# Kernel optimization log

Hardware: AMD Instinct MI355X
Metric: run time of the kernel (lower is better)

The kernel has to match this reference:

```python
import jax, jax.numpy as jnp
import numpy as np

N_NODES = 100000
N_EDGES = 1600000
D_IN = 128
D_HID = 64


def setup_inputs() -> dict:
    key = jax.random.key(0)
    k1, k2, k3, k4 = jax.random.split(key, 4)
    x = jax.random.normal(k1, (N_NODES, D_IN), dtype=jnp.float32)
    edge_index = jax.random.randint(k2, (2, N_EDGES), 0, N_NODES, dtype=jnp.int64)
    W1 = jax.random.normal(k3, (D_IN, D_HID), dtype=jnp.float32) / np.sqrt(D_IN)
    b1 = jnp.zeros((D_HID,), dtype=jnp.float32)
    W2 = jax.random.normal(k4, (D_HID, 1), dtype=jnp.float32) / np.sqrt(D_HID)
    b2 = jnp.zeros((1,), dtype=jnp.float32)
    return {"x": x, "edge_index": edge_index, "W1": W1, "b1": b1, "W2": W2, "b2": b2}


def _gcn_layer(x, W, b, src, dst, norm, n):
    # PyG GCNConv: linear transform, then normalized scatter-add aggregation, then bias
    h = x @ W                                   # [N, d_out]
    msg = h[src] * norm[:, None]                # gather + edge-weight   [E', d_out]
    out = jax.ops.segment_sum(msg, dst, num_segments=n)  # scatter-add
    return out + b


def reference(x, edge_index, W1, b1, W2, b2):
    n = x.shape[0]
    loops = jnp.arange(n, dtype=edge_index.dtype)
    src = jnp.concatenate([edge_index[0], loops])  # self-loops added (GCN default)
    dst = jnp.concatenate([edge_index[1], loops])
    # symmetric normalization: deg^{-1/2}[src] * deg^{-1/2}[dst]
    deg = jax.ops.segment_sum(jnp.ones(dst.shape, x.dtype), dst, num_segments=n)
    dis = jnp.where(deg > 0, jax.lax.rsqrt(jnp.maximum(deg, 1e-12)), 0.0)
    norm = dis[src] * dis[dst]
    h = jax.nn.relu(_gcn_layer(x, W1, b1, src, dst, norm, n))
    y = _gcn_layer(h, W2, b2, src, dst, norm, n)   # [N, 1]
    # ConstantPad1d((0, num_node_features-1), 0) -> [N, D_IN]
    return jnp.pad(y, ((0, 0), (0, x.shape[1] - 1)))
```

## Files before the change

### kernel.cpp

```cpp
#include <hip/hip_runtime.h>

#define N_NODES 100000
#define N_EDGES 1600000
#define D_IN 128
#define D_HID 64

#define BKT_SHIFT 8
#define BKT_NODES 256
#define NB 391
#define NBLK 392
#define SLOT 32
#define SEG4 (SLOT / 4)
#define REG4 (NBLK * SEG4)
#define BKT_CAP 5120
#define OVF_CAP 8192

typedef __attribute__((ext_vector_type(8))) short bf16x8;
typedef __attribute__((ext_vector_type(4))) float f32x4;

__device__ __forceinline__ unsigned short f2b(float f) {
    union { float f; unsigned u; } c; c.f = f;
    unsigned r = (c.u + 0x7FFFu + ((c.u >> 16) & 1u)) >> 16;
    return (unsigned short)r;
}
__device__ __forceinline__ float blo(unsigned u) { return __uint_as_float(u << 16); }
__device__ __forceinline__ float bhi(unsigned u) { return __uint_as_float(u & 0xffff0000u); }

__global__ __launch_bounds__(256) void k_prep(const float* __restrict__ W1,
                                              unsigned short* __restrict__ w1t,
                                              int* __restrict__ ovf_cnt) {
    int t = blockIdx.x * 256 + threadIdx.x;
    if (t == 0) ovf_cnt[0] = 0;
    int k = t >> 6, f = t & 63;
    w1t[f * D_IN + k] = f2b(W1[t]);
}

__global__ __launch_bounds__(256) void k_escatter(const int* __restrict__ src,
                                                  const int* __restrict__ dst,
                                                  int* __restrict__ pairs,
                                                  int* __restrict__ cnt_blk,
                                                  int* __restrict__ ovf_cnt,
                                                  int2* __restrict__ ovf, int E) {
    __shared__ int lcur[NB];
    int tid = threadIdx.x;
    for (int t = tid; t < NB; t += 256) lcur[t] = 0;
    __syncthreads();
    int chunk = (E + NBLK - 1) / NBLK;
    int beg = blockIdx.x * chunk;
    int end = min(beg + chunk, E);
    for (int e = beg + tid; e < end; e += 256) {
        int d = dst[e], s = src[e];
        int bk = d >> BKT_SHIFT;
        int slot = atomicAdd(&lcur[bk], 1);
        if (slot < SLOT)
            pairs[(bk * NBLK + blockIdx.x) * SLOT + slot] = (s << BKT_SHIFT) | (d & (BKT_NODES - 1));
        else {
            int o = atomicAdd(ovf_cnt, 1);
            if (o < OVF_CAP) ovf[o] = make_int2(s, d);
        }
    }
    __syncthreads();
    for (int t = tid; t < NB; t += 256)
        cnt_blk[t * NBLK + blockIdx.x] = min(lcur[t], SLOT);
}

__global__ __launch_bounds__(256) void k_bsort(const uint4* __restrict__ pairs4,
                                               const int* __restrict__ cnt_blk,
                                               const int* __restrict__ ovf_cnt,
                                               const int2* __restrict__ ovf,
                                               int* __restrict__ srcs_sorted,
                                               int* __restrict__ row_start,
                                               int* __restrict__ row_end,
                                               float* __restrict__ dis, int n) {
    __shared__ int segc[NBLK];
    __shared__ int cnt[BKT_NODES];
    __shared__ int exc[BKT_NODES];
    __shared__ int sorted[BKT_CAP];
    __shared__ int nE_sh;
    int b = blockIdx.x;
    int tid = threadIdx.x;
    int node0 = b << BKT_SHIFT;
    int ocnt = min(ovf_cnt[0], OVF_CAP);
    const uint4* region = pairs4 + (size_t)b * REG4;

    for (int i = tid; i < NBLK; i += 256) segc[i] = cnt_blk[b * NBLK + i];
    cnt[tid] = 0;
    __syncthreads();

    for (int i4 = tid; i4 < REG4; i4 += 256) {
        uint4 v = region[i4];
        int c = segc[i4 >> 3];
        int k = (i4 & 7) * 4;
        if (k < c)     atomicAdd(&cnt[v.x & (BKT_NODES - 1)], 1);
        if (k + 1 < c) atomicAdd(&cnt[v.y & (BKT_NODES - 1)], 1);
        if (k + 2 < c) atomicAdd(&cnt[v.z & (BKT_NODES - 1)], 1);
        if (k + 3 < c) atomicAdd(&cnt[v.w & (BKT_NODES - 1)], 1);
    }
    for (int k = tid; k < ocnt; k += 256) {
        int2 e = ovf[k];
        if ((e.y >> BKT_SHIFT) == b) atomicAdd(&cnt[e.y & (BKT_NODES - 1)], 1);
    }
    __syncthreads();

    if (tid < 64) {
        int run = 0;
        for (int c = 0; c < BKT_NODES; c += 64) {
            int v = cnt[c + tid];
            int inc = v;
            for (int off = 1; off < 64; off <<= 1) {
                int t2 = __shfl_up(inc, off);
                if (tid >= off) inc += t2;
            }
            exc[c + tid] = run + inc - v;
            run += __shfl(inc, 63);
        }
        if (tid == 63) nE_sh = run;
    }
    __syncthreads();

    int node = node0 + tid;
    if (node < n) {
        int rs = b * BKT_CAP + exc[tid];
        row_start[node] = rs;
        row_end[node] = rs + cnt[tid];
        dis[node] = rsqrtf((float)cnt[tid] + 1.0f);
    }
    int nE = nE_sh;
    __syncthreads();
    cnt[tid] = exc[tid];
    __syncthreads();

    for (int i4 = tid; i4 < REG4; i4 += 256) {
        uint4 v = region[i4];
        int c = segc[i4 >> 3];
        int k = (i4 & 7) * 4;
        if (k < c)     { int p = atomicAdd(&cnt[v.x & (BKT_NODES - 1)], 1); sorted[p] = v.x >> BKT_SHIFT; }
        if (k + 1 < c) { int p = atomicAdd(&cnt[v.y & (BKT_NODES - 1)], 1); sorted[p] = v.y >> BKT_SHIFT; }
        if (k + 2 < c) { int p = atomicAdd(&cnt[v.z & (BKT_NODES - 1)], 1); sorted[p] = v.z >> BKT_SHIFT; }
        if (k + 3 < c) { int p = atomicAdd(&cnt[v.w & (BKT_NODES - 1)], 1); sorted[p] = v.w >> BKT_SHIFT; }
    }
    for (int k = tid; k < ocnt; k += 256) {
        int2 e = ovf[k];
        if ((e.y >> BKT_SHIFT) == b) {
            int p = atomicAdd(&cnt[e.y & (BKT_NODES - 1)], 1);
            sorted[p] = e.x;
        }
    }
    __syncthreads();

    int gbase = b * BKT_CAP;
    for (int k = tid; k < nE; k += 256)
        srcs_sorted[gbase + k] = sorted[k];
}

#define LS 136
__global__ __launch_bounds__(256) void k_gemm1(const float* __restrict__ x,
                                               const uint4* __restrict__ w1t4,
                                               const float* __restrict__ dis,
                                               unsigned short* __restrict__ h1s, int n) {
    __shared__ unsigned short xs[64 * LS];
    __shared__ unsigned short ws[64 * LS];
    int tid = threadIdx.x;
    int node0 = blockIdx.x * 64;

#pragma unroll
    for (int it = 0; it < 4; ++it) {
        int e = tid + it * 256;
        int f = e >> 4, c = e & 15;
        *(uint4*)&ws[f * LS + c * 8] = w1t4[e];
    }
#pragma unroll
    for (int it = 0; it < 8; ++it) {
        int e4 = tid + it * 256;
        int node = e4 >> 5;
        int k = (e4 & 31) * 4;
        float4 v = make_float4(0.f, 0.f, 0.f, 0.f);
        if (node0 + node < n)
            v = ((const float4*)x)[((size_t)(node0 + node) * D_IN + k) >> 2];
        uint2 u;
        u.x = (unsigned)f2b(v.x) | ((unsigned)f2b(v.y) << 16);
        u.y = (unsigned)f2b(v.z) | ((unsigned)f2b(v.w) << 16);
        *(uint2*)&xs[node * LS + k] = u;
    }
    __syncthreads();

    int wv = tid >> 6;
    int lane = tid & 63;
    int m16 = lane & 15;
    int q = lane >> 4;

    bf16x8 afrag[4];
#pragma unroll
    for (int ks = 0; ks < 4; ++ks)
        afrag[ks] = *(const bf16x8*)&xs[(wv * 16 + m16) * LS + ks * 32 + q * 8];

    f32x4 acc[4];
#pragma unroll
    for (int ft = 0; ft < 4; ++ft) acc[ft] = (f32x4){0.f, 0.f, 0.f, 0.f};

#pragma unroll
    for (int ft = 0; ft < 4; ++ft)
#pragma unroll
        for (int ks = 0; ks < 4; ++ks) {
            bf16x8 bfrag = *(const bf16x8*)&ws[(ft * 16 + m16) * LS + ks * 32 + q * 8];
            acc[ft] = __builtin_amdgcn_mfma_f32_16x16x32_bf16(afrag[ks], bfrag, acc[ft], 0, 0, 0);
        }

#pragma unroll
    for (int r = 0; r < 4; ++r) {
        int node = node0 + wv * 16 + q * 4 + r;
        if (node < n) {
            float d = dis[node];
#pragma unroll
            for (int ft = 0; ft < 4; ++ft)
                h1s[(size_t)node * D_HID + ft * 16 + m16] = f2b(acc[ft][r] * d);
        }
    }
}

__global__ __launch_bounds__(256) void k_gather1(const int* __restrict__ srcs,
                                                 const int* __restrict__ row_start,
                                                 const int* __restrict__ row_end,
                                                 const float* __restrict__ dis,
                                                 const uint4* __restrict__ h4,
                                                 const float* __restrict__ b1,
                                                 const float* __restrict__ W2,
                                                 float* __restrict__ zd, int n) {
    int i = blockIdx.x * 8 + (threadIdx.x >> 5);
    int lane = threadIdx.x & 63;
    int g = (lane >> 3) & 3;
    int m8 = lane & 7;
    float dd = dis[i];

    float a0, a1, a2, a3, a4, a5, a6, a7;
    {
        uint4 u = h4[(unsigned)i * 8u + m8];
        float w = (g == 0) ? 1.f : 0.f;
        a0 = w * blo(u.x); a1 = w * bhi(u.x);
        a2 = w * blo(u.y); a3 = w * bhi(u.y);
        a4 = w * blo(u.z); a5 = w * bhi(u.z);
        a6 = w * blo(u.w); a7 = w * bhi(u.w);
    }

#define ACC(u) { a0 += blo(u.x); a1 += bhi(u.x); a2 += blo(u.y); a3 += bhi(u.y); \
                 a4 += blo(u.z); a5 += bhi(u.z); a6 += blo(u.w); a7 += bhi(u.w); }
    int end = row_end[i];
    int j = row_start[i] + g;
    for (; j + 4 < end; j += 8) {
        int s0 = srcs[j];
        int s1 = srcs[j + 4];
        uint4 u0 = h4[(unsigned)s0 * 8u + m8];
        uint4 u1 = h4[(unsigned)s1 * 8u + m8];
        ACC(u0); ACC(u1);
    }
    if (j < end) {
        int s0 = srcs[j];
        uint4 u0 = h4[(unsigned)s0 * 8u + m8];
        ACC(u0);
    }
#undef ACC

#pragma unroll
    for (int off = 8; off < 32; off <<= 1) {
        a0 += __shfl_xor(a0, off); a1 += __shfl_xor(a1, off);
        a2 += __shfl_xor(a2, off); a3 += __shfl_xor(a3, off);
        a4 += __shfl_xor(a4, off); a5 += __shfl_xor(a5, off);
        a6 += __shfl_xor(a6, off); a7 += __shfl_xor(a7, off);
    }
    float4 ba = ((const float4*)b1)[m8 * 2];
    float4 bb = ((const float4*)b1)[m8 * 2 + 1];
    float4 wa = ((const float4*)W2)[m8 * 2];
    float4 wb = ((const float4*)W2)[m8 * 2 + 1];
    float v = fmaxf(fmaf(dd, a0, ba.x), 0.f) * wa.x + fmaxf(fmaf(dd, a1, ba.y), 0.f) * wa.y
            + fmaxf(fmaf(dd, a2, ba.z), 0.f) * wa.z + fmaxf(fmaf(dd, a3, ba.w), 0.f) * wa.w
            + fmaxf(fmaf(dd, a4, bb.x), 0.f) * wb.x + fmaxf(fmaf(dd, a5, bb.y), 0.f) * wb.y
            + fmaxf(fmaf(dd, a6, bb.z), 0.f) * wb.z + fmaxf(fmaf(dd, a7, bb.w), 0.f) * wb.w;
#pragma unroll
    for (int off = 1; off < 8; off <<= 1) v += __shfl_xor(v, off);
    if ((lane & 31) == 0) zd[i] = v * dd;
}

__global__ __launch_bounds__(256) void k_gather2(const int* __restrict__ srcs,
                                                 const int* __restrict__ row_start,
                                                 const int* __restrict__ row_end,
                                                 const float* __restrict__ dis,
                                                 const float* __restrict__ zd,
                                                 const float* __restrict__ b2,
                                                 float* __restrict__ out, int n) {
    int i = blockIdx.x * 8 + (threadIdx.x >> 5);
    int l = threadIdx.x & 31;
    float acc = 0.f;
    int beg = row_start[i], end = row_end[i];
    for (int j = beg + l; j < end; j += 32)
        acc += zd[srcs[j]];
#pragma unroll
    for (int off = 1; off < 32; off <<= 1) acc += __shfl_xor(acc, off);
    float y = (acc + zd[i]) * dis[i] + b2[0];
    float4 v = make_float4(0.f, 0.f, 0.f, 0.f);
    if (l == 0) v.x = y;
    ((float4*)out)[(size_t)i * 32 + l] = v;
}

extern "C" void kernel_launch(void* const* d_in, const int* in_sizes, int n_in,
                              void* d_out, int out_size, void* d_ws, size_t ws_size,
                              hipStream_t stream) {
    const float* x  = (const float*)d_in[0];
    const int*   ei = (const int*)d_in[1];
    const float* W1 = (const float*)d_in[2];
    const float* b1 = (const float*)d_in[3];
    const float* W2 = (const float*)d_in[4];
    const float* b2 = (const float*)d_in[5];
    float* out = (float*)d_out;

    const int n = N_NODES;
    const int E = N_EDGES;
    const int* src = ei;
    const int* dst = ei + E;

    int* pairs       = (int*)d_ws;
    int* cnt_blk     = pairs + (size_t)NB * NBLK * SLOT;
    int* srcs_sorted = cnt_blk + (size_t)NB * NBLK;
    int* row_start   = srcs_sorted + (size_t)NB * BKT_CAP;
    int* row_end     = row_start + n;
    int* ovf_cnt     = row_end + n;
    int2* ovf        = (int2*)(ovf_cnt + 4);
    float* dis       = (float*)(ovf + OVF_CAP);
    unsigned short* h1s = (unsigned short*)(dis + n);
    unsigned short* w1t = h1s + (size_t)n * D_HID;
    float* zd        = (float*)(w1t + D_IN * D_HID);

    k_prep<<<32, 256, 0, stream>>>(W1, w1t, ovf_cnt);
    k_escatter<<<NBLK, 256, 0, stream>>>(src, dst, pairs, cnt_blk, ovf_cnt, ovf, E);
    k_bsort<<<NB, 256, 0, stream>>>((const uint4*)pairs, cnt_blk, ovf_cnt, ovf,
                                    srcs_sorted, row_start, row_end, dis, n);

    k_gemm1<<<(n + 63) / 64, 256, 0, stream>>>(x, (const uint4*)w1t, dis, h1s, n);

    k_gather1<<<(n + 7) / 8, 256, 0, stream>>>(srcs_sorted, row_start, row_end, dis,
                                               (const uint4*)h1s, b1, W2, zd, n);
    k_gather2<<<(n + 7) / 8, 256, 0, stream>>>(srcs_sorted, row_start, row_end, dis,
                                               zd, b2, out, n);
}
```

Baseline: 213.2 us.

## Stage bucket pairs compactly in LDS once and fold W1 prep into scatter

The bucket sort kernel now prefix-sums the per-block segment counts and reads the padded global pair region once, compacting only valid entries into a shared staging array. Both the count and placement passes then iterate over that dense array, so the second global read and the idle padded-slot work are gone. The separate W1 transpose kernel is merged into the edge scatter kernel, and the overflow counter is reset with a memset, which removes one kernel launch. In exchange the kernel uses an extra 20KB of LDS, which may reduce occupancy.

```diff
diff --git a/kernel.cpp b/kernel.cpp
--- a/kernel.cpp
+++ b/kernel.cpp
@@ -26,23 +26,21 @@
 __device__ __forceinline__ float blo(unsigned u) { return __uint_as_float(u << 16); }
 __device__ __forceinline__ float bhi(unsigned u) { return __uint_as_float(u & 0xffff0000u); }
 
-__global__ __launch_bounds__(256) void k_prep(const float* __restrict__ W1,
-                                              unsigned short* __restrict__ w1t,
-                                              int* __restrict__ ovf_cnt) {
-    int t = blockIdx.x * 256 + threadIdx.x;
-    if (t == 0) ovf_cnt[0] = 0;
-    int k = t >> 6, f = t & 63;
-    w1t[f * D_IN + k] = f2b(W1[t]);
-}
-
 __global__ __launch_bounds__(256) void k_escatter(const int* __restrict__ src,
                                                   const int* __restrict__ dst,
+                                                  const float* __restrict__ W1,
+                                                  unsigned short* __restrict__ w1t,
                                                   int* __restrict__ pairs,
                                                   int* __restrict__ cnt_blk,
                                                   int* __restrict__ ovf_cnt,
                                                   int2* __restrict__ ovf, int E) {
     __shared__ int lcur[NB];
     int tid = threadIdx.x;
+    if (blockIdx.x < 32) {
+        int t = blockIdx.x * 256 + tid;
+        int k = t >> 6, f = t & 63;
+        w1t[f * D_IN + k] = f2b(W1[t]);
+    }
     for (int t = tid; t < NB; t += 256) lcur[t] = 0;
     __syncthreads();
     int chunk = (E + NBLK - 1) / NBLK;
@@ -73,8 +71,10 @@
                                                int* __restrict__ row_end,
                                                float* __restrict__ dis, int n) {
     __shared__ int segc[NBLK];
+    __shared__ int segb[NBLK];
     __shared__ int cnt[BKT_NODES];
     __shared__ int exc[BKT_NODES];
+    __shared__ int staged[BKT_CAP];
     __shared__ int sorted[BKT_CAP];
     __shared__ int nE_sh;
     int b = blockIdx.x;
@@ -87,15 +87,41 @@
     cnt[tid] = 0;
     __syncthreads();
 
+    if (tid < 64) {
+        int run = 0;
+        for (int c = 0; c < NBLK; c += 64) {
+            int idx = c + tid;
+            int v = (idx < NBLK) ? segc[idx] : 0;
+            int inc = v;
+            for (int off = 1; off < 64; off <<= 1) {
+                int t2 = __shfl_up(inc, off);
+                if (tid >= off) inc += t2;
+            }
+            if (idx < NBLK) segb[idx] = run + inc - v;
+            run += __shfl(inc, 63);
+        }
+        if (tid == 63) nE_sh = run;
+    }
+    __syncthreads();
+
     for (int i4 = tid; i4 < REG4; i4 += 256) {
-        uint4 v = region[i4];
-        int c = segc[i4 >> 3];
+        int seg = i4 >> 3;
+        int c = segc[seg];
         int k = (i4 & 7) * 4;
-        if (k < c)     atomicAdd(&cnt[v.x & (BKT_NODES - 1)], 1);
-        if (k + 1 < c) atomicAdd(&cnt[v.y & (BKT_NODES - 1)], 1);
-        if (k + 2 < c) atomicAdd(&cnt[v.z & (BKT_NODES - 1)], 1);
-        if (k + 3 < c) atomicAdd(&cnt[v.w & (BKT_NODES - 1)], 1);
-    }
+        if (k < c) {
+            uint4 v = region[i4];
+            int base = segb[seg] + k;
+            if (base < BKT_CAP)                  staged[base]     = v.x;
+            if (k + 1 < c && base + 1 < BKT_CAP) staged[base + 1] = v.y;
+            if (k + 2 < c && base + 2 < BKT_CAP) staged[base + 2] = v.z;
+            if (k + 3 < c && base + 3 < BKT_CAP) staged[base + 3] = v.w;
+        }
+    }
+    __syncthreads();
+    int nE = min(nE_sh, BKT_CAP);
+
+    for (int k = tid; k < nE; k += 256)
+        atomicAdd(&cnt[staged[k] & (BKT_NODES - 1)], 1);
     for (int k = tid; k < ocnt; k += 256) {
         int2 e = ovf[k];
         if ((e.y >> BKT_SHIFT) == b) atomicAdd(&cnt[e.y & (BKT_NODES - 1)], 1);
@@ -114,30 +140,25 @@
             exc[c + tid] = run + inc - v;
             run += __shfl(inc, 63);
         }
-        if (tid == 63) nE_sh = run;
     }
     __syncthreads();
 
     int node = node0 + tid;
+    int tot = exc[BKT_NODES - 1] + cnt[BKT_NODES - 1];
     if (node < n) {
         int rs = b * BKT_CAP + exc[tid];
         row_start[node] = rs;
         row_end[node] = rs + cnt[tid];
         dis[node] = rsqrtf((float)cnt[tid] + 1.0f);
     }
-    int nE = nE_sh;
     __syncthreads();
     cnt[tid] = exc[tid];
     __syncthreads();
 
-    for (int i4 = tid; i4 < REG4; i4 += 256) {
-        uint4 v = region[i4];
-        int c = segc[i4 >> 3];
-        int k = (i4 & 7) * 4;
-        if (k < c)     { int p = atomicAdd(&cnt[v.x & (BKT_NODES - 1)], 1); sorted[p] = v.x >> BKT_SHIFT; }
-        if (k + 1 < c) { int p = atomicAdd(&cnt[v.y & (BKT_NODES - 1)], 1); sorted[p] = v.y >> BKT_SHIFT; }
-        if (k + 2 < c) { int p = atomicAdd(&cnt[v.z & (BKT_NODES - 1)], 1); sorted[p] = v.z >> BKT_SHIFT; }
-        if (k + 3 < c) { int p = atomicAdd(&cnt[v.w & (BKT_NODES - 1)], 1); sorted[p] = v.w >> BKT_SHIFT; }
+    for (int k = tid; k < nE; k += 256) {
+        int pk = staged[k];
+        int p = atomicAdd(&cnt[pk & (BKT_NODES - 1)], 1);
+        sorted[p] = pk >> BKT_SHIFT;
     }
     for (int k = tid; k < ocnt; k += 256) {
         int2 e = ovf[k];
@@ -149,7 +170,8 @@
     __syncthreads();
 
     int gbase = b * BKT_CAP;
-    for (int k = tid; k < nE; k += 256)
+    int nTot = min(tot, BKT_CAP);
+    for (int k = tid; k < nTot; k += 256)
         srcs_sorted[gbase + k] = sorted[k];
 }
 
@@ -329,8 +351,8 @@
     unsigned short* w1t = h1s + (size_t)n * D_HID;
     float* zd        = (float*)(w1t + D_IN * D_HID);
 
-    k_prep<<<32, 256, 0, stream>>>(W1, w1t, ovf_cnt);
-    k_escatter<<<NBLK, 256, 0, stream>>>(src, dst, pairs, cnt_blk, ovf_cnt, ovf, E);
+    hipMemsetAsync(ovf_cnt, 0, 4, stream);
+    k_escatter<<<NBLK, 256, 0, stream>>>(src, dst, W1, w1t, pairs, cnt_blk, ovf_cnt, ovf, E);
     k_bsort<<<NB, 256, 0, stream>>>((const uint4*)pairs, cnt_blk, ovf_cnt, ovf,
                                     srcs_sorted, row_start, row_end, dis, n);
 
```

Result: slower. 222.1 us (+4.2%).

## Fuse edge scatter and GEMM1 into one launch, apply source norm in gather

Applied to the files above, without the earlier changes.

Merges the edge-scatter kernel and the first dense GEMM into a single heterogeneous launch, so the GEMM blocks run alongside the scatter blocks. Because the GEMM now runs before degrees are known, it stores unscaled h1, and the gather kernel multiplies each neighbour row by dis[src] with an extra scalar load per edge. The W1 transpose/prep kernel is dropped: every GEMM block converts W1 itself, and the overflow counter is reset with a memset. Launch count and serialization go down, but the gather does extra random loads and each GEMM block does redundant W1 conversion with strided shared-memory stores.

```diff
diff --git a/kernel.cpp b/kernel.cpp
--- a/kernel.cpp
+++ b/kernel.cpp
@@ -9,6 +9,7 @@
 #define BKT_NODES 256
 #define NB 391
 #define NBLK 392
+#define GBLK 1563
 #define SLOT 32
 #define SEG4 (SLOT / 4)
 #define REG4 (NBLK * SEG4)
@@ -26,42 +27,98 @@
 __device__ __forceinline__ float blo(unsigned u) { return __uint_as_float(u << 16); }
 __device__ __forceinline__ float bhi(unsigned u) { return __uint_as_float(u & 0xffff0000u); }
 
-__global__ __launch_bounds__(256) void k_prep(const float* __restrict__ W1,
-                                              unsigned short* __restrict__ w1t,
-                                              int* __restrict__ ovf_cnt) {
-    int t = blockIdx.x * 256 + threadIdx.x;
-    if (t == 0) ovf_cnt[0] = 0;
-    int k = t >> 6, f = t & 63;
-    w1t[f * D_IN + k] = f2b(W1[t]);
-}
-
-__global__ __launch_bounds__(256) void k_escatter(const int* __restrict__ src,
-                                                  const int* __restrict__ dst,
-                                                  int* __restrict__ pairs,
-                                                  int* __restrict__ cnt_blk,
-                                                  int* __restrict__ ovf_cnt,
-                                                  int2* __restrict__ ovf, int E) {
+#define LS 136
+__global__ __launch_bounds__(256) void k_build(const int* __restrict__ src,
+                                               const int* __restrict__ dst,
+                                               const float* __restrict__ x,
+                                               const float* __restrict__ W1,
+                                               int* __restrict__ pairs,
+                                               int* __restrict__ cnt_blk,
+                                               int* __restrict__ ovf_cnt,
+                                               int2* __restrict__ ovf,
+                                               unsigned short* __restrict__ h1,
+                                               int E, int n) {
     __shared__ int lcur[NB];
+    __shared__ unsigned short xs[64 * LS];
+    __shared__ unsigned short ws[64 * LS];
     int tid = threadIdx.x;
-    for (int t = tid; t < NB; t += 256) lcur[t] = 0;
-    __syncthreads();
-    int chunk = (E + NBLK - 1) / NBLK;
-    int beg = blockIdx.x * chunk;
-    int end = min(beg + chunk, E);
-    for (int e = beg + tid; e < end; e += 256) {
-        int d = dst[e], s = src[e];
-        int bk = d >> BKT_SHIFT;
-        int slot = atomicAdd(&lcur[bk], 1);
-        if (slot < SLOT)
-            pairs[(bk * NBLK + blockIdx.x) * SLOT + slot] = (s << BKT_SHIFT) | (d & (BKT_NODES - 1));
-        else {
-            int o = atomicAdd(ovf_cnt, 1);
-            if (o < OVF_CAP) ovf[o] = make_int2(s, d);
-        }
-    }
-    __syncthreads();
-    for (int t = tid; t < NB; t += 256)
-        cnt_blk[t * NBLK + blockIdx.x] = min(lcur[t], SLOT);
+
+    if (blockIdx.x < NBLK) {
+        for (int t = tid; t < NB; t += 256) lcur[t] = 0;
+        __syncthreads();
+        int chunk = (E + NBLK - 1) / NBLK;
+        int beg = blockIdx.x * chunk;
+        int end = min(beg + chunk, E);
+        for (int e = beg + tid; e < end; e += 256) {
+            int d = dst[e], s = src[e];
+            int bk = d >> BKT_SHIFT;
+            int slot = atomicAdd(&lcur[bk], 1);
+            if (slot < SLOT)
+                pairs[(bk * NBLK + blockIdx.x) * SLOT + slot] = (s << BKT_SHIFT) | (d & (BKT_NODES - 1));
+            else {
+                int o = atomicAdd(ovf_cnt, 1);
+                if (o < OVF_CAP) ovf[o] = make_int2(s, d);
+            }
+        }
+        __syncthreads();
+        for (int t = tid; t < NB; t += 256)
+            cnt_blk[t * NBLK + blockIdx.x] = min(lcur[t], SLOT);
+        return;
+    }
+
+    int node0 = (blockIdx.x - NBLK) * 64;
+#pragma unroll
+    for (int it = 0; it < 32; ++it) {
+        int e = tid + it * 256;
+        int k = e >> 6, f = e & 63;
+        ws[f * LS + k] = f2b(W1[e]);
+    }
+#pragma unroll
+    for (int it = 0; it < 8; ++it) {
+        int e4 = tid + it * 256;
+        int node = e4 >> 5;
+        int k = (e4 & 31) * 4;
+        float4 v = make_float4(0.f, 0.f, 0.f, 0.f);
+        if (node0 + node < n)
+            v = ((const float4*)x)[((size_t)(node0 + node) * D_IN + k) >> 2];
+        uint2 u;
+        u.x = (unsigned)f2b(v.x) | ((unsigned)f2b(v.y) << 16);
+        u.y = (unsigned)f2b(v.z) | ((unsigned)f2b(v.w) << 16);
+        *(uint2*)&xs[node * LS + k] = u;
+    }
+    __syncthreads();
+
+    int wv = tid >> 6;
+    int lane = tid & 63;
+    int m16 = lane & 15;
+    int q = lane >> 4;
+
+    bf16x8 afrag[4];
+#pragma unroll
+    for (int ks = 0; ks < 4; ++ks)
+        afrag[ks] = *(const bf16x8*)&xs[(wv * 16 + m16) * LS + ks * 32 + q * 8];
+
+    f32x4 acc[4];
+#pragma unroll
+    for (int ft = 0; ft < 4; ++ft) acc[ft] = (f32x4){0.f, 0.f, 0.f, 0.f};
+
+#pragma unroll
+    for (int ft = 0; ft < 4; ++ft)
+#pragma unroll
+        for (int ks = 0; ks < 4; ++ks) {
+            bf16x8 bfrag = *(const bf16x8*)&ws[(ft * 16 + m16) * LS + ks * 32 + q * 8];
+            acc[ft] = __builtin_amdgcn_mfma_f32_16x16x32_bf16(afrag[ks], bfrag, acc[ft], 0, 0, 0);
+        }
+
+#pragma unroll
+    for (int r = 0; r < 4; ++r) {
+        int node = node0 + wv * 16 + q * 4 + r;
+        if (node < n) {
+#pragma unroll
+            for (int ft = 0; ft < 4; ++ft)
+                h1[(size_t)node * D_HID + ft * 16 + m16] = f2b(acc[ft][r]);
+        }
+    }
 }
 
 __global__ __launch_bounds__(256) void k_bsort(const uint4* __restrict__ pairs4,
@@ -76,7 +133,6 @@
     __shared__ int cnt[BKT_NODES];
     __shared__ int exc[BKT_NODES];
     __shared__ int sorted[BKT_CAP];
-    __shared__ int nE_sh;
     int b = blockIdx.x;
     int tid = threadIdx.x;
     int node0 = b << BKT_SHIFT;
@@ -114,10 +170,10 @@
             exc[c + tid] = run + inc - v;
             run += __shfl(inc, 63);
         }
-        if (tid == 63) nE_sh = run;
-    }
-    __syncthreads();
-
+    }
+    __syncthreads();
+
+    int tot = min(exc[BKT_NODES - 1] + cnt[BKT_NODES - 1], BKT_CAP);
     int node = node0 + tid;
     if (node < n) {
         int rs = b * BKT_CAP + exc[tid];
@@ -125,7 +181,6 @@
         row_end[node] = rs + cnt[tid];
         dis[node] = rsqrtf((float)cnt[tid] + 1.0f);
     }
-    int nE = nE_sh;
     __syncthreads();
     cnt[tid] = exc[tid];
     __syncthreads();
@@ -149,73 +204,8 @@
     __syncthreads();
 
     int gbase = b * BKT_CAP;
-    for (int k = tid; k < nE; k += 256)
+    for (int k = tid; k < tot; k += 256)
         srcs_sorted[gbase + k] = sorted[k];
-}
-
-#define LS 136
-__global__ __launch_bounds__(256) void k_gemm1(const float* __restrict__ x,
-                                               const uint4* __restrict__ w1t4,
-                                               const float* __restrict__ dis,
-                                               unsigned short* __restrict__ h1s, int n) {
-    __shared__ unsigned short xs[64 * LS];
-    __shared__ unsigned short ws[64 * LS];
-    int tid = threadIdx.x;
-    int node0 = blockIdx.x * 64;
-
-#pragma unroll
-    for (int it = 0; it < 4; ++it) {
-        int e = tid + it * 256;
-        int f = e >> 4, c = e & 15;
-        *(uint4*)&ws[f * LS + c * 8] = w1t4[e];
-    }
-#pragma unroll
-    for (int it = 0; it < 8; ++it) {
-        int e4 = tid + it * 256;
-        int node = e4 >> 5;
-        int k = (e4 & 31) * 4;
-        float4 v = make_float4(0.f, 0.f, 0.f, 0.f);
-        if (node0 + node < n)
-            v = ((const float4*)x)[((size_t)(node0 + node) * D_IN + k) >> 2];
-        uint2 u;
-        u.x = (unsigned)f2b(v.x) | ((unsigned)f2b(v.y) << 16);
-        u.y = (unsigned)f2b(v.z) | ((unsigned)f2b(v.w) << 16);
-        *(uint2*)&xs[node * LS + k] = u;
-    }
-    __syncthreads();
-
-    int wv = tid >> 6;
-    int lane = tid & 63;
-    int m16 = lane & 15;
-    int q = lane >> 4;
-
-    bf16x8 afrag[4];
-#pragma unroll
-    for (int ks = 0; ks < 4; ++ks)
-        afrag[ks] = *(const bf16x8*)&xs[(wv * 16 + m16) * LS + ks * 32 + q * 8];
-
-    f32x4 acc[4];
-#pragma unroll
-    for (int ft = 0; ft < 4; ++ft) acc[ft] = (f32x4){0.f, 0.f, 0.f, 0.f};
-
-#pragma unroll
-    for (int ft = 0; ft < 4; ++ft)
-#pragma unroll
-        for (int ks = 0; ks < 4; ++ks) {
-            bf16x8 bfrag = *(const bf16x8*)&ws[(ft * 16 + m16) * LS + ks * 32 + q * 8];
-            acc[ft] = __builtin_amdgcn_mfma_f32_16x16x32_bf16(afrag[ks], bfrag, acc[ft], 0, 0, 0);
-        }
-
-#pragma unroll
-    for (int r = 0; r < 4; ++r) {
-        int node = node0 + wv * 16 + q * 4 + r;
-        if (node < n) {
-            float d = dis[node];
-#pragma unroll
-            for (int ft = 0; ft < 4; ++ft)
-                h1s[(size_t)node * D_HID + ft * 16 + m16] = f2b(acc[ft][r] * d);
-        }
-    }
 }
 
 __global__ __launch_bounds__(256) void k_gather1(const int* __restrict__ srcs,
@@ -235,30 +225,34 @@
     float a0, a1, a2, a3, a4, a5, a6, a7;
     {
         uint4 u = h4[(unsigned)i * 8u + m8];
-        float w = (g == 0) ? 1.f : 0.f;
+        float w = (g == 0) ? dd : 0.f;
         a0 = w * blo(u.x); a1 = w * bhi(u.x);
         a2 = w * blo(u.y); a3 = w * bhi(u.y);
         a4 = w * blo(u.z); a5 = w * bhi(u.z);
         a6 = w * blo(u.w); a7 = w * bhi(u.w);
     }
 
-#define ACC(u) { a0 += blo(u.x); a1 += bhi(u.x); a2 += blo(u.y); a3 += bhi(u.y); \
-                 a4 += blo(u.z); a5 += bhi(u.z); a6 += blo(u.w); a7 += bhi(u.w); }
+#define ACCW(U, W) { a0 = fmaf(W, blo(U.x), a0); a1 = fmaf(W, bhi(U.x), a1); \
+                     a2 = fmaf(W, blo(U.y), a2); a3 = fmaf(W, bhi(U.y), a3); \
+                     a4 = fmaf(W, blo(U.z), a4); a5 = fmaf(W, bhi(U.z), a5); \
+                     a6 = fmaf(W, blo(U.w), a6); a7 = fmaf(W, bhi(U.w), a7); }
     int end = row_end[i];
     int j = row_start[i] + g;
     for (; j + 4 < end; j += 8) {
         int s0 = srcs[j];
         int s1 = srcs[j + 4];
+        float w0 = dis[s0], w1 = dis[s1];
         uint4 u0 = h4[(unsigned)s0 * 8u + m8];
         uint4 u1 = h4[(unsigned)s1 * 8u + m8];
-        ACC(u0); ACC(u1);
+        ACCW(u0, w0); ACCW(u1, w1);
     }
     if (j < end) {
         int s0 = srcs[j];
+        float w0 = dis[s0];
         uint4 u0 = h4[(unsigned)s0 * 8u + m8];
-        ACC(u0);
-    }
-#undef ACC
+        ACCW(u0, w0);
+    }
+#undef ACCW
 
 #pragma unroll
     for (int off = 8; off < 32; off <<= 1) {
@@ -325,19 +319,16 @@
     int* ovf_cnt     = row_end + n;
     int2* ovf        = (int2*)(ovf_cnt + 4);
     float* dis       = (float*)(ovf + OVF_CAP);
-    unsigned short* h1s = (unsigned short*)(dis + n);
-    unsigned short* w1t = h1s + (size_t)n * D_HID;
-    float* zd        = (float*)(w1t + D_IN * D_HID);
-
-    k_prep<<<32, 256, 0, stream>>>(W1, w1t, ovf_cnt);
-    k_escatter<<<NBLK, 256, 0, stream>>>(src, dst, pairs, cnt_blk, ovf_cnt, ovf, E);
+    unsigned short* h1 = (unsigned short*)(dis + n);
+    float* zd        = (float*)(h1 + (size_t)n * D_HID);
+
+    (void)hipMemsetAsync(ovf_cnt, 0, 4, stream);
+    k_build<<<NBLK + GBLK, 256, 0, stream>>>(src, dst, x, W1, pairs, cnt_blk,
+                                             ovf_cnt, ovf, h1, E, n);
     k_bsort<<<NB, 256, 0, stream>>>((const uint4*)pairs, cnt_blk, ovf_cnt, ovf,
                                     srcs_sorted, row_start, row_end, dis, n);
-
-    k_gemm1<<<(n + 63) / 64, 256, 0, stream>>>(x, (const uint4*)w1t, dis, h1s, n);
-
     k_gather1<<<(n + 7) / 8, 256, 0, stream>>>(srcs_sorted, row_start, row_end, dis,
-                                               (const uint4*)h1s, b1, W2, zd, n);
+                                               (const uint4*)h1, b1, W2, zd, n);
     k_gather2<<<(n + 7) / 8, 256, 0, stream>>>(srcs_sorted, row_start, row_end, dis,
                                                zd, b2, out, n);
 }
```

New measurement: 226.8 us. 6.4% more time.
